# Kernel tuning notes

Hardware: AMD Instinct MI355X
Metric: run time of the kernel (lower is better)

Reference implementation:

```python
import jax, jax.numpy as jnp
import numpy as np

DT_MIN, DT_MAX = 1e-3, 0.1
DT_RANK, D_STATE = 64, 16


def setup_inputs() -> dict:
    key = jax.random.key(0)
    ks = jax.random.split(key, 8)
    B, L, D_MODEL, D_INNER = 2, 4096, 1024, 2048
    s = 0.02
    return {
        "x": jax.random.normal(ks[0], (B, L, D_MODEL), jnp.float32),
        "W_in": jax.random.normal(ks[1], (D_MODEL, 2 * D_INNER), jnp.float32) * s,
        "W_xproj": jax.random.normal(ks[2], (D_INNER, DT_RANK + 2 * D_STATE), jnp.float32) * s,
        "W_dt": jax.random.normal(ks[3], (DT_RANK, D_INNER), jnp.float32) * s,
        "b_dt": jax.random.normal(ks[4], (D_INNER,), jnp.float32) * s,
        "A_log": jnp.log(jax.random.uniform(ks[5], (D_INNER, D_STATE), jnp.float32) + 0.5),
        "D": jnp.ones((D_INNER,), jnp.float32),
        "W_out": jax.random.normal(ks[6], (D_INNER, D_MODEL), jnp.float32) * s,
    }


def _selective_scan(xp, delta, A, Bm, Cm):
    # xp, delta: [B, L, d_inner]; Bm, Cm: [B, L, d_state]; A: [d_inner, d_state]
    batch, L, d_inner = xp.shape
    d_state = A.shape[1]

    def step(h, inp):
        x_t, dt_t, B_t, C_t = inp  # [B,di], [B,di], [B,ds], [B,ds]
        A_bar = 1.0 + A[None] * dt_t[..., None]            # [B, di, ds]
        B_bar = B_t[:, None, :] * dt_t[..., None]          # [B, di, ds]
        h = A_bar * h + B_bar * x_t[..., None]             # [B, di, ds]
        y_t = jnp.sum(C_t[:, None, :] * h, axis=-1)        # [B, di]
        return h, y_t

    h0 = jnp.zeros((batch, d_inner, d_state), xp.dtype)
    xs = (
        jnp.swapaxes(xp, 0, 1),
        jnp.swapaxes(delta, 0, 1),
        jnp.swapaxes(Bm, 0, 1),
        jnp.swapaxes(Cm, 0, 1),
    )
    _, ys = jax.lax.scan(step, h0, xs)  # ys: [L, B, d_inner]
    return jnp.swapaxes(ys, 0, 1)


def reference(x, W_in, W_xproj, W_dt, b_dt, A_log, D, W_out):
    xz = x @ W_in
    xp, z = jnp.split(xz, 2, axis=-1)                      # [B,L,d_inner] each
    x_dbl = xp @ W_xproj
    dlt, Bm, Cm = jnp.split(x_dbl, [DT_RANK, DT_RANK + D_STATE], axis=-1)
    delta = jnp.clip(jax.nn.softplus(dlt @ W_dt + b_dt), DT_MIN, DT_MAX)
    A = -jnp.exp(A_log)
    y = _selective_scan(xp, delta, A, Bm, Cm)
    y = y + D[None, None, :] * xp
    y = y * jax.nn.silu(z)
    return y @ W_out
```

## Files before the change

### kernel.cpp

```cpp
#include <hip/hip_runtime.h>
#include <cstdint>
#include <cstddef>

typedef unsigned short u16;
typedef __attribute__((ext_vector_type(8))) short bf16x8;
typedef __attribute__((ext_vector_type(4))) float f32x4;

__device__ __forceinline__ float bf2f(u16 u) {
  unsigned v = ((unsigned)u) << 16;
  return __builtin_bit_cast(float, v);
}
__device__ __forceinline__ u16 f2bf(float f) {
  unsigned u = __builtin_bit_cast(unsigned, f);
  u = (u + 0x7FFFu + ((u >> 16) & 1u)) >> 16;
  return (u16)u;
}

__device__ __forceinline__ void gload16(const void* g, void* l) {
  __builtin_amdgcn_global_load_lds(
      (const __attribute__((address_space(1))) void*)g,
      (__attribute__((address_space(3))) void*)l,
      16, 0, 0);
}

__device__ __forceinline__ int swz(int lb) { return lb ^ (((lb >> 7) & 7) << 4); }

__global__ __launch_bounds__(256) void f32_to_bf16_kernel(
    const float* __restrict__ in, u16* __restrict__ out, int n) {
  int i = (blockIdx.x * 256 + threadIdx.x) * 4;
  if (i < n) {
    float4 v = *(const float4*)(in + i);
    ushort4 o;
    o.x = f2bf(v.x); o.y = f2bf(v.y); o.z = f2bf(v.z); o.w = f2bf(v.w);
    *(ushort4*)(out + i) = o;
  }
}

__global__ void transpose_f32_bf16T_kernel(
    const float* __restrict__ in, u16* __restrict__ out, int R, int C) {
  __shared__ float tile[32][33];
  const int bx = blockIdx.x * 32;
  const int by = blockIdx.y * 32;
  const int tx = threadIdx.x, ty = threadIdx.y;
#pragma unroll
  for (int i = 0; i < 32; i += 8)
    tile[ty + i][tx] = in[(size_t)(by + ty + i) * C + bx + tx];
  __syncthreads();
#pragma unroll
  for (int i = 0; i < 32; i += 8)
    out[(size_t)(bx + ty + i) * R + by + tx] = f2bf(tile[tx][ty + i]);
}

template <int BN, int EPI>
__global__ __launch_bounds__(512, 2) void gemm256(
    const u16* __restrict__ Ap, const u16* __restrict__ Btp,
    int M, int N, int K, int gx,
    void* __restrict__ o0, void* __restrict__ o1) {
  constexpr int NFR = BN / 64;
  constexpr int NFH = NFR / 2;
  constexpr int B_ISS = BN / 64;
  constexpr int WN = BN / 4;
  constexpr int AREG = 32768;
  constexpr int BUFSZ = AREG + BN * 128;
  __shared__ __align__(1024) char smem[2 * BUFSZ];

  const int tid = threadIdx.x;
  const int wid = tid >> 6, lane = tid & 63;
  const int wr = wid >> 2, wc = wid & 3;
  const int l16 = lane & 15, lk = lane >> 4;

  const int nwg = gridDim.x, bid = blockIdx.x;
  const int rb = (bid & 7) * (nwg >> 3) + (bid >> 3);
  const int bx = rb % gx, by = rb / gx;
  const int m0 = by * 256, n0 = bx * BN;

  const u16* gA[4];
  const u16* gB[B_ISS];
#pragma unroll
  for (int i = 0; i < 4; ++i) {
    int lb = swz(i * 8192 + tid * 16);
    gA[i] = Ap + (size_t)(m0 + (lb >> 7)) * K + ((lb & 127) >> 1);
  }
#pragma unroll
  for (int i = 0; i < B_ISS; ++i) {
    int lb = swz(i * 8192 + tid * 16);
    gB[i] = Btp + (size_t)(n0 + (lb >> 7)) * K + ((lb & 127) >> 1);
  }

  auto stageA = [&](int kt, int h) {
    char* dst = smem + (kt & 1) * BUFSZ + (wid << 10);
    gload16(gA[2 * h] + kt * 64, dst + (2 * h) * 8192);
    gload16(gA[2 * h + 1] + kt * 64, dst + (2 * h + 1) * 8192);
  };
  auto stageB = [&](int kt, int h) {
    char* dst = smem + (kt & 1) * BUFSZ + AREG + (wid << 10);
    if constexpr (B_ISS == 4) {
      gload16(gB[2 * h] + kt * 64, dst + (2 * h) * 8192);
      gload16(gB[2 * h + 1] + kt * 64, dst + (2 * h + 1) * 8192);
    } else {
      gload16(gB[h] + kt * 64, dst + h * 8192);
    }
  };

  auto offA = [&](int f, int kk) {
    return swz((wr * 128 + f * 16 + l16) * 128 + kk * 64 + lk * 16);
  };
  auto offB = [&](int n, int kk) {
    return swz((wc * WN + n * 16 + l16) * 128 + kk * 64 + lk * 16);
  };

  f32x4 acc[8][NFR];
#pragma unroll
  for (int f = 0; f < 8; ++f)
#pragma unroll
    for (int n = 0; n < NFR; ++n) {
      f32x4 z = {0.f, 0.f, 0.f, 0.f};
      acc[f][n] = z;
    }

  const int NT = K >> 6;
  stageA(0, 0); stageA(0, 1); stageB(0, 0); stageB(0, 1);
  stageA(1, 0);
  asm volatile("s_waitcnt vmcnt(2)" ::: "memory");
  __builtin_amdgcn_s_barrier();

  for (int kt = 0; kt < NT; ++kt) {
    const char* bufA = smem + (kt & 1) * BUFSZ;
    const char* bufB = bufA + AREG;
    bf16x8 af[4][2], bh[2][NFH][2];

#pragma unroll
    for (int j = 0; j < 4; ++j)
#pragma unroll
      for (int kk = 0; kk < 2; ++kk)
        af[j][kk] = *(const bf16x8*)(bufA + offA(j, kk));
#pragma unroll
    for (int j = 0; j < NFH; ++j)
#pragma unroll
      for (int kk = 0; kk < 2; ++kk)
        bh[0][j][kk] = *(const bf16x8*)(bufB + offB(j, kk));
    if (kt + 1 < NT) stageA(kt + 1, 1);
    __builtin_amdgcn_s_barrier();
    asm volatile("s_waitcnt lgkmcnt(0)" ::: "memory");
    __builtin_amdgcn_sched_barrier(0);
    __builtin_amdgcn_s_setprio(1);
#pragma unroll
    for (int j = 0; j < 4; ++j)
#pragma unroll
      for (int n2 = 0; n2 < NFH; ++n2)
#pragma unroll
        for (int kk = 0; kk < 2; ++kk)
          acc[j][n2] = __builtin_amdgcn_mfma_f32_16x16x32_bf16(
              af[j][kk], bh[0][n2][kk], acc[j][n2], 0, 0, 0);
    __builtin_amdgcn_s_setprio(0);
    __builtin_amdgcn_s_barrier();

#pragma unroll
    for (int j = 0; j < NFH; ++j)
#pragma unroll
      for (int kk = 0; kk < 2; ++kk)
        bh[1][j][kk] = *(const bf16x8*)(bufB + offB(NFH + j, kk));
    if (kt + 1 < NT) stageB(kt + 1, 0);
    __builtin_amdgcn_s_barrier();
    asm volatile("s_waitcnt lgkmcnt(0)" ::: "memory");
    __builtin_amdgcn_sched_barrier(0);
    __builtin_amdgcn_s_setprio(1);
#pragma unroll
    for (int j = 0; j < 4; ++j)
#pragma unroll
      for (int n2 = 0; n2 < NFH; ++n2)
#pragma unroll
        for (int kk = 0; kk < 2; ++kk)
          acc[j][NFH + n2] = __builtin_amdgcn_mfma_f32_16x16x32_bf16(
              af[j][kk], bh[1][n2][kk], acc[j][NFH + n2], 0, 0, 0);
    __builtin_amdgcn_s_setprio(0);
    __builtin_amdgcn_s_barrier();

#pragma unroll
    for (int j = 0; j < 4; ++j)
#pragma unroll
      for (int kk = 0; kk < 2; ++kk)
        af[j][kk] = *(const bf16x8*)(bufA + offA(4 + j, kk));
    if (kt + 1 < NT) stageB(kt + 1, 1);
    __builtin_amdgcn_s_barrier();
    asm volatile("s_waitcnt lgkmcnt(0)" ::: "memory");
    __builtin_amdgcn_sched_barrier(0);
    __builtin_amdgcn_s_setprio(1);
#pragma unroll
    for (int j = 0; j < 4; ++j)
#pragma unroll
      for (int n2 = 0; n2 < NFH; ++n2)
#pragma unroll
        for (int kk = 0; kk < 2; ++kk)
          acc[4 + j][NFH + n2] = __builtin_amdgcn_mfma_f32_16x16x32_bf16(
              af[j][kk], bh[1][n2][kk], acc[4 + j][NFH + n2], 0, 0, 0);
    __builtin_amdgcn_s_setprio(0);
    __builtin_amdgcn_s_barrier();

    if (kt + 2 < NT) {
      stageA(kt + 2, 0);
      asm volatile("s_waitcnt vmcnt(2)" ::: "memory");
    } else if (kt + 1 < NT) {
      asm volatile("s_waitcnt vmcnt(0)" ::: "memory");
    }
    __builtin_amdgcn_s_barrier();
    __builtin_amdgcn_s_setprio(1);
#pragma unroll
    for (int j = 0; j < 4; ++j)
#pragma unroll
      for (int n2 = 0; n2 < NFH; ++n2)
#pragma unroll
        for (int kk = 0; kk < 2; ++kk)
          acc[4 + j][n2] = __builtin_amdgcn_mfma_f32_16x16x32_bf16(
              af[j][kk], bh[0][n2][kk], acc[4 + j][n2], 0, 0, 0);
    __builtin_amdgcn_s_setprio(0);
    __builtin_amdgcn_s_barrier();
  }

#pragma unroll
  for (int f = 0; f < 8; ++f) {
#pragma unroll
    for (int n = 0; n < NFR; ++n) {
#pragma unroll
      for (int rr = 0; rr < 4; ++rr) {
        const int row = m0 + wr * 128 + f * 16 + lk * 4 + rr;
        const int col = n0 + wc * WN + n * 16 + l16;
        float v = acc[f][n][rr];
        if constexpr (EPI == 0) {
          if (col < 2048) {
            ((u16*)o0)[(size_t)row * 2048 + col] = f2bf(v);
          } else {
            float sv = v / (1.f + __expf(-v));
            ((u16*)o1)[(size_t)row * 2048 + (col - 2048)] = f2bf(sv);
          }
        } else {
          ((float*)o0)[(size_t)row * (size_t)N + col] = v;
        }
      }
    }
  }
}

template <int BN, int NR, int EPI>
__global__ __launch_bounds__(256) void gemm_bt(
    const u16* __restrict__ A, const u16* __restrict__ Bt,
    int M, int N, int K, int KS,
    void* __restrict__ o0, const float* __restrict__ bias) {
  constexpr int BM = 128, BK = 32, MR = 4;
  __shared__ __align__(16) u16 As[BM * BK];
  __shared__ __align__(16) u16 Bs[BN * BK];
  const int tid = threadIdx.x;
  const int wid = tid >> 6, lane = tid & 63;
  const int wr = wid >> 1, wc = wid & 1;
  const int m0 = blockIdx.y * BM, n0 = blockIdx.x * BN;
  const int l16 = lane & 15, lk = lane >> 4;

  f32x4 acc[MR][NR];
#pragma unroll
  for (int m = 0; m < MR; ++m)
#pragma unroll
    for (int n = 0; n < NR; ++n) {
      f32x4 z = {0.f, 0.f, 0.f, 0.f};
      acc[m][n] = z;
    }

  constexpr int CH_A = (BM * BK * 2) / 1024;
  constexpr int CH_B = (BN * BK * 2) / 1024;

  const int kbeg = blockIdx.z * KS, kend = kbeg + KS;
  for (int k0 = kbeg; k0 < kend; k0 += BK) {
    for (int c = wid; c < CH_A; c += 4) {
      int off = c * 1024 + lane * 16;
      int e = off >> 1;
      int m = e >> 5, kk = e & 31;
      gload16(A + (size_t)(m0 + m) * K + (k0 + kk), (char*)As + off);
    }
    for (int c = wid; c < CH_B; c += 4) {
      int off = c * 1024 + lane * 16;
      int e = off >> 1;
      int n = e >> 5, kk = e & 31;
      gload16(Bt + (size_t)(n0 + n) * K + (k0 + kk), (char*)Bs + off);
    }
    __syncthreads();
    bf16x8 af[MR], bfr[NR];
#pragma unroll
    for (int m = 0; m < MR; ++m)
      af[m] = *(const bf16x8*)(As + (wr * 64 + m * 16 + l16) * BK + lk * 8);
#pragma unroll
    for (int n = 0; n < NR; ++n)
      bfr[n] = *(const bf16x8*)(Bs + (wc * (NR * 16) + n * 16 + l16) * BK + lk * 8);
#pragma unroll
    for (int m = 0; m < MR; ++m)
#pragma unroll
      for (int n = 0; n < NR; ++n)
        acc[m][n] = __builtin_amdgcn_mfma_f32_16x16x32_bf16(af[m], bfr[n], acc[m][n], 0, 0, 0);
    __syncthreads();
  }

#pragma unroll
  for (int m = 0; m < MR; ++m) {
#pragma unroll
    for (int n = 0; n < NR; ++n) {
#pragma unroll
      for (int r = 0; r < 4; ++r) {
        const int row = m0 + wr * 64 + m * 16 + (lane >> 4) * 4 + r;
        const int col = n0 + wc * (NR * 16) + n * 16 + (lane & 15);
        float v = acc[m][n][r];
        if constexpr (EPI == 2) {
          v += bias[col];
          float sp = (v > 20.f) ? v : log1pf(__expf(v));
          sp = fminf(fmaxf(sp, 1e-3f), 0.1f);
          ((u16*)o0)[(size_t)row * 2048 + col] = f2bf(sp);
        } else {
          ((float*)o0)[((size_t)blockIdx.z * M + row) * 96 + col] = v;
        }
      }
    }
  }
}

__global__ __launch_bounds__(256) void reduce_xdbl(
    const float* __restrict__ part, u16* __restrict__ dlt,
    float* __restrict__ Bc, float* __restrict__ Cc) {
  int idx = blockIdx.x * 256 + threadIdx.x;
  int row = idx / 24, c4 = idx % 24;
  const float* p = part + (size_t)row * 96 + c4 * 4;
  f32x4 v = *(const f32x4*)p;
#pragma unroll
  for (int z = 1; z < 4; ++z)
    v += *(const f32x4*)(p + (size_t)z * 8192 * 96);
  int col = c4 * 4;
  if (col < 64) {
    ushort4 o;
    o.x = f2bf(v[0]); o.y = f2bf(v[1]); o.z = f2bf(v[2]); o.w = f2bf(v[3]);
    *(ushort4*)(dlt + (size_t)row * 64 + col) = o;
  } else if (col < 80) {
    *(f32x4*)(Bc + (size_t)row * 16 + (col - 64)) = v;
  } else {
    *(f32x4*)(Cc + (size_t)row * 16 + (col - 80)) = v;
  }
}

template <int TC>
__global__ __launch_bounds__(256) void scan_pass1(
    const u16* __restrict__ xp, const u16* __restrict__ dt,
    const float* __restrict__ Bc, const float* __restrict__ A_log,
    float* __restrict__ P, float* __restrict__ Q, int NC) {
  const int di = blockIdx.x * 256 + threadIdx.x;
  const int c = blockIdx.y, b = blockIdx.z;
  __shared__ __align__(16) float Bs[TC * 16];
  {
    const float* src = Bc + (size_t)(b * 4096 + c * TC) * 16;
    for (int i = threadIdx.x; i < TC * 4; i += 256)
      *(float4*)(Bs + i * 4) = *(const float4*)(src + i * 4);
  }
  float A[16], h[16], Pp[16];
#pragma unroll
  for (int s = 0; s < 16; ++s) {
    A[s] = -__expf(A_log[di * 16 + s]);
    h[s] = 0.f;
    Pp[s] = 1.f;
  }
  __syncthreads();
  size_t gidx = (size_t)(b * 4096 + c * TC) * 2048 + di;
  for (int t = 0; t < TC; ++t, gidx += 2048) {
    float xv = bf2f(xp[gidx]), dv = bf2f(dt[gidx]);
    float dvx = dv * xv;
#pragma unroll
    for (int q = 0; q < 4; ++q) {
      f32x4 bv = ((const f32x4*)(Bs + t * 16))[q];
#pragma unroll
      for (int j = 0; j < 4; ++j) {
        int s = q * 4 + j;
        float abar = fmaf(A[s], dv, 1.f);
        h[s] = fmaf(abar, h[s], bv[j] * dvx);
        Pp[s] *= abar;
      }
    }
  }
  const size_t obase = ((size_t)(b * NC + c) * 16) * 2048 + di;
#pragma unroll
  for (int s = 0; s < 16; ++s) {
    P[obase + (size_t)s * 2048] = Pp[s];
    Q[obase + (size_t)s * 2048] = h[s];
  }
}

__global__ __launch_bounds__(256) void scan_pass2(
    const float* __restrict__ P, const float* __restrict__ Q,
    float* __restrict__ Hin, int NC) {
  const int di = blockIdx.x * 256 + threadIdx.x;
  const int s = blockIdx.y, b = blockIdx.z;
  float hin = 0.f;
  const size_t idx0 = ((size_t)(b * NC) * 16 + s) * 2048 + di;
#pragma unroll 8
  for (int c = 0; c < NC; ++c) {
    size_t idx = idx0 + (size_t)c * (16 * 2048);
    Hin[idx] = hin;
    hin = fmaf(P[idx], hin, Q[idx]);
  }
}

template <int TC>
__global__ __launch_bounds__(256) void scan_pass3(
    const u16* __restrict__ xp, const u16* __restrict__ dt,
    const u16* __restrict__ zs, const float* __restrict__ Bc,
    const float* __restrict__ Cc, const float* __restrict__ A_log,
    const float* __restrict__ Dv, const float* __restrict__ Hin,
    u16* __restrict__ Y, int NC) {
  const int di = blockIdx.x * 256 + threadIdx.x;
  const int c = blockIdx.y, b = blockIdx.z;
  __shared__ __align__(16) float Bs[TC * 16], Cs[TC * 16];
  {
    const float* srcB = Bc + (size_t)(b * 4096 + c * TC) * 16;
    const float* srcC = Cc + (size_t)(b * 4096 + c * TC) * 16;
    for (int i = threadIdx.x; i < TC * 4; i += 256) {
      *(float4*)(Bs + i * 4) = *(const float4*)(srcB + i * 4);
      *(float4*)(Cs + i * 4) = *(const float4*)(srcC + i * 4);
    }
  }
  float A[16], h[16];
  const size_t hbase = ((size_t)(b * NC + c) * 16) * 2048 + di;
#pragma unroll
  for (int s = 0; s < 16; ++s) {
    A[s] = -__expf(A_log[di * 16 + s]);
    h[s] = Hin[hbase + (size_t)s * 2048];
  }
  const float Dg = Dv[di];
  __syncthreads();
  size_t gidx = (size_t)(b * 4096 + c * TC) * 2048 + di;
  for (int t = 0; t < TC; ++t, gidx += 2048) {
    float xv = bf2f(xp[gidx]), dv = bf2f(dt[gidx]), zv = bf2f(zs[gidx]);
    float dvx = dv * xv;
    float y = 0.f;
#pragma unroll
    for (int q = 0; q < 4; ++q) {
      f32x4 bv = ((const f32x4*)(Bs + t * 16))[q];
      f32x4 cv = ((const f32x4*)(Cs + t * 16))[q];
#pragma unroll
      for (int j = 0; j < 4; ++j) {
        int s = q * 4 + j;
        float abar = fmaf(A[s], dv, 1.f);
        h[s] = fmaf(abar, h[s], bv[j] * dvx);
        y = fmaf(cv[j], h[s], y);
      }
    }
    float yo = fmaf(Dg, xv, y) * zv;
    Y[gidx] = f2bf(yo);
  }
}

extern "C" void kernel_launch(void* const* d_in, const int* in_sizes, int n_in,
                              void* d_out, int out_size, void* d_ws, size_t ws_size,
                              hipStream_t stream) {
  (void)in_sizes; (void)n_in; (void)out_size; (void)ws_size;
  const float* x       = (const float*)d_in[0];
  const float* W_in    = (const float*)d_in[1];
  const float* W_xproj = (const float*)d_in[2];
  const float* W_dt    = (const float*)d_in[3];
  const float* b_dt    = (const float*)d_in[4];
  const float* A_log   = (const float*)d_in[5];
  const float* Dv      = (const float*)d_in[6];
  const float* W_out   = (const float*)d_in[7];
  float* out = (float*)d_out;

  constexpr size_t MB = 1ull << 20;
  char* ws = (char*)d_ws;
  constexpr size_t O_XP    = 0;
  constexpr size_t O_ZS    = 32 * MB;
  constexpr size_t O_DELTA = 64 * MB;
  constexpr size_t O_BC    = 96 * MB;
  constexpr size_t O_CC    = O_BC + 512 * 1024;
  constexpr size_t O_WOUTT = 97 * MB;
  constexpr size_t O_Y     = 101 * MB;
  constexpr size_t O_XB    = 133 * MB;
  constexpr size_t O_WINT  = 149 * MB;
  constexpr size_t O_WXT   = 157 * MB;
  constexpr size_t O_WDTT  = O_WXT + 393216;
  constexpr size_t O_DLT   = O_WDTT + 262144;
  constexpr size_t O_P     = 133 * MB;
  constexpr size_t O_Q     = 149 * MB;
  constexpr size_t O_HIN   = 165 * MB;
  constexpr size_t O_XDP   = O_P;

  u16* xb    = (u16*)(ws + O_XB);
  u16* WinT  = (u16*)(ws + O_WINT);
  u16* WxT   = (u16*)(ws + O_WXT);
  u16* WdtT  = (u16*)(ws + O_WDTT);
  u16* WoutT = (u16*)(ws + O_WOUTT);
  u16* xpb   = (u16*)(ws + O_XP);
  u16* zsb   = (u16*)(ws + O_ZS);
  u16* dltb  = (u16*)(ws + O_DLT);
  float* Bcf = (float*)(ws + O_BC);
  float* Ccf = (float*)(ws + O_CC);
  u16* delb  = (u16*)(ws + O_DELTA);
  u16* Yb    = (u16*)(ws + O_Y);
  float* Pf  = (float*)(ws + O_P);
  float* Qf  = (float*)(ws + O_Q);
  float* Hin = (float*)(ws + O_HIN);
  float* xdp = (float*)(ws + O_XDP);

  dim3 tb(32, 8);
  f32_to_bf16_kernel<<<8192 * 1024 / 1024, 256, 0, stream>>>(x, xb, 8192 * 1024);
  transpose_f32_bf16T_kernel<<<dim3(4096 / 32, 1024 / 32), tb, 0, stream>>>(W_in, WinT, 1024, 4096);
  transpose_f32_bf16T_kernel<<<dim3(96 / 32, 2048 / 32), tb, 0, stream>>>(W_xproj, WxT, 2048, 96);
  transpose_f32_bf16T_kernel<<<dim3(2048 / 32, 64 / 32), tb, 0, stream>>>(W_dt, WdtT, 64, 2048);
  transpose_f32_bf16T_kernel<<<dim3(1024 / 32, 2048 / 32), tb, 0, stream>>>(W_out, WoutT, 2048, 1024);

  gemm256<256, 0><<<512, 512, 0, stream>>>(
      xb, WinT, 8192, 4096, 1024, 16, xpb, zsb);
  gemm_bt<96, 3, 4><<<dim3(1, 8192 / 128, 4), 256, 0, stream>>>(
      xpb, WxT, 8192, 96, 2048, 512, xdp, nullptr);
  reduce_xdbl<<<8192 * 24 / 256, 256, 0, stream>>>(xdp, dltb, Bcf, Ccf);
  gemm_bt<128, 4, 2><<<dim3(2048 / 128, 8192 / 128, 1), 256, 0, stream>>>(
      dltb, WdtT, 8192, 2048, 64, 64, delb, b_dt);

  constexpr int NC = 64, TC = 64;
  scan_pass1<TC><<<dim3(8, NC, 2), 256, 0, stream>>>(
      xpb, delb, Bcf, A_log, Pf, Qf, NC);
  scan_pass2<<<dim3(8, 16, 2), 256, 0, stream>>>(Pf, Qf, Hin, NC);
  scan_pass3<TC><<<dim3(8, NC, 2), 256, 0, stream>>>(
      xpb, delb, zsb, Bcf, Ccf, A_log, Dv, Hin, Yb, NC);

  gemm256<128, 3><<<256, 512, 0, stream>>>(
      Yb, WoutT, 8192, 1024, 2048, 8, out, nullptr);
}
```

Baseline: 329.9 us.

## Reorganize GEMM LDS staging so tile halves load as independent groups

Remaps the A and B tile rows in shared memory so each half of the tile (A row groups, B column halves) is loaded as a separate group. The prefetch schedule changes so the next tile's first halves are issued early and second halves later, with vmcnt waits placed after the MFMA phases rather than in a separate stage. The intent is finer-grained overlap of global-to-LDS loads with compute and the removal of one barrier per iteration. The risk is that the new row interleaving and wait counts must exactly match the issue order, or the kernel will read stale data.

```diff
diff --git a/kernel.cpp b/kernel.cpp
--- a/kernel.cpp
+++ b/kernel.cpp
@@ -59,9 +59,12 @@
   constexpr int NFR = BN / 64;
   constexpr int NFH = NFR / 2;
   constexpr int B_ISS = BN / 64;
+  constexpr int BH = B_ISS / 2;
   constexpr int WN = BN / 4;
+  constexpr int HSH = (BN == 256) ? 5 : 4;
   constexpr int AREG = 32768;
-  constexpr int BUFSZ = AREG + BN * 128;
+  constexpr int BREG = BN * 128;
+  constexpr int BUFSZ = AREG + BREG;
   __shared__ __align__(1024) char smem[2 * BUFSZ];
 
   const int tid = threadIdx.x;
@@ -84,29 +87,31 @@
 #pragma unroll
   for (int i = 0; i < B_ISS; ++i) {
     int lb = swz(i * 8192 + tid * 16);
-    gB[i] = Btp + (size_t)(n0 + (lb >> 7)) * K + ((lb & 127) >> 1);
+    int rl = lb >> 7;
+    int half = (rl >= BN / 2) ? 1 : 0;
+    int r = rl & (BN / 2 - 1);
+    int n = ((r >> HSH) << (HSH + 1)) + (half << HSH) + (r & ((1 << HSH) - 1));
+    gB[i] = Btp + (size_t)(n0 + n) * K + ((lb & 127) >> 1);
   }
 
   auto stageA = [&](int kt, int h) {
     char* dst = smem + (kt & 1) * BUFSZ + (wid << 10);
-    gload16(gA[2 * h] + kt * 64, dst + (2 * h) * 8192);
-    gload16(gA[2 * h + 1] + kt * 64, dst + (2 * h + 1) * 8192);
+    gload16(gA[h] + kt * 64, dst + h * 8192);
+    gload16(gA[h + 2] + kt * 64, dst + (h + 2) * 8192);
   };
   auto stageB = [&](int kt, int h) {
     char* dst = smem + (kt & 1) * BUFSZ + AREG + (wid << 10);
-    if constexpr (B_ISS == 4) {
-      gload16(gB[2 * h] + kt * 64, dst + (2 * h) * 8192);
-      gload16(gB[2 * h + 1] + kt * 64, dst + (2 * h + 1) * 8192);
-    } else {
-      gload16(gB[h] + kt * 64, dst + h * 8192);
-    }
+#pragma unroll
+    for (int j = 0; j < BH; ++j)
+      gload16(gB[h * BH + j] + kt * 64, dst + (h * BH + j) * 8192);
   };
 
   auto offA = [&](int f, int kk) {
     return swz((wr * 128 + f * 16 + l16) * 128 + kk * 64 + lk * 16);
   };
-  auto offB = [&](int n, int kk) {
-    return swz((wc * WN + n * 16 + l16) * 128 + kk * 64 + lk * 16);
+  auto offB = [&](int nf, int kk) {
+    int rl = (nf >= NFH ? BN / 2 : 0) + wc * (WN / 2) + (nf % NFH) * 16 + l16;
+    return swz(rl * 128 + kk * 64 + lk * 16);
   };
 
   f32x4 acc[8][NFR];
@@ -119,9 +124,9 @@
     }
 
   const int NT = K >> 6;
-  stageA(0, 0); stageA(0, 1); stageB(0, 0); stageB(0, 1);
-  stageA(1, 0);
-  asm volatile("s_waitcnt vmcnt(2)" ::: "memory");
+  stageA(0, 0); stageB(0, 0); stageA(0, 1); stageB(0, 1);
+  if constexpr (BH == 2) asm volatile("s_waitcnt vmcnt(4)" ::: "memory");
+  else                   asm volatile("s_waitcnt vmcnt(3)" ::: "memory");
   __builtin_amdgcn_s_barrier();
 
   for (int kt = 0; kt < NT; ++kt) {
@@ -139,7 +144,7 @@
 #pragma unroll
       for (int kk = 0; kk < 2; ++kk)
         bh[0][j][kk] = *(const bf16x8*)(bufB + offB(j, kk));
-    if (kt + 1 < NT) stageA(kt + 1, 1);
+    if (kt + 1 < NT) stageA(kt + 1, 0);
     __builtin_amdgcn_s_barrier();
     asm volatile("s_waitcnt lgkmcnt(0)" ::: "memory");
     __builtin_amdgcn_sched_barrier(0);
@@ -153,6 +158,8 @@
           acc[j][n2] = __builtin_amdgcn_mfma_f32_16x16x32_bf16(
               af[j][kk], bh[0][n2][kk], acc[j][n2], 0, 0, 0);
     __builtin_amdgcn_s_setprio(0);
+    if (kt + 1 < NT) asm volatile("s_waitcnt vmcnt(2)" ::: "memory");
+    else             asm volatile("s_waitcnt vmcnt(0)" ::: "memory");
     __builtin_amdgcn_s_barrier();
 
 #pragma unroll
@@ -181,7 +188,7 @@
 #pragma unroll
       for (int kk = 0; kk < 2; ++kk)
         af[j][kk] = *(const bf16x8*)(bufA + offA(4 + j, kk));
-    if (kt + 1 < NT) stageB(kt + 1, 1);
+    if (kt + 1 < NT) { stageA(kt + 1, 1); stageB(kt + 1, 1); }
     __builtin_amdgcn_s_barrier();
     asm volatile("s_waitcnt lgkmcnt(0)" ::: "memory");
     __builtin_amdgcn_sched_barrier(0);
@@ -197,13 +204,6 @@
     __builtin_amdgcn_s_setprio(0);
     __builtin_amdgcn_s_barrier();
 
-    if (kt + 2 < NT) {
-      stageA(kt + 2, 0);
-      asm volatile("s_waitcnt vmcnt(2)" ::: "memory");
-    } else if (kt + 1 < NT) {
-      asm volatile("s_waitcnt vmcnt(0)" ::: "memory");
-    }
-    __builtin_amdgcn_s_barrier();
     __builtin_amdgcn_s_setprio(1);
 #pragma unroll
     for (int j = 0; j < 4; ++j)
@@ -214,6 +214,10 @@
           acc[4 + j][n2] = __builtin_amdgcn_mfma_f32_16x16x32_bf16(
               af[j][kk], bh[0][n2][kk], acc[4 + j][n2], 0, 0, 0);
     __builtin_amdgcn_s_setprio(0);
+    if (kt + 1 < NT) {
+      if constexpr (BH == 2) asm volatile("s_waitcnt vmcnt(4)" ::: "memory");
+      else                   asm volatile("s_waitcnt vmcnt(3)" ::: "memory");
+    }
     __builtin_amdgcn_s_barrier();
   }
 
```

New measurement: 328.0 us. No clear change (-0.6%).

## Load GEMM B operand directly to registers and single-buffer A in LDS

Applied to the files above, without the earlier changes.

The gemm256 kernel stops staging the B (weight) tile through LDS. Each wave now loads its B fragments straight from global memory into registers, ping-ponged across two register sets by unrolling the k loop by two. A is single-buffered in a 32KB LDS region with split staging and new vmcnt waits, and block rasterization changes to column-major over M tiles (gy). This cuts LDS footprint and LDS traffic, but adds register pressure and uncoalesced-ish global loads for B, and it assumes NT is even.

```diff
diff --git a/kernel.cpp b/kernel.cpp
--- a/kernel.cpp
+++ b/kernel.cpp
@@ -54,15 +54,13 @@
 template <int BN, int EPI>
 __global__ __launch_bounds__(512, 2) void gemm256(
     const u16* __restrict__ Ap, const u16* __restrict__ Btp,
-    int M, int N, int K, int gx,
+    int M, int N, int K, int gy,
     void* __restrict__ o0, void* __restrict__ o1) {
   constexpr int NFR = BN / 64;
   constexpr int NFH = NFR / 2;
-  constexpr int B_ISS = BN / 64;
+  constexpr int BL = 2 * NFH;
   constexpr int WN = BN / 4;
-  constexpr int AREG = 32768;
-  constexpr int BUFSZ = AREG + BN * 128;
-  __shared__ __align__(1024) char smem[2 * BUFSZ];
+  __shared__ __align__(1024) char smem[32768];
 
   const int tid = threadIdx.x;
   const int wid = tid >> 6, lane = tid & 63;
@@ -71,43 +69,31 @@
 
   const int nwg = gridDim.x, bid = blockIdx.x;
   const int rb = (bid & 7) * (nwg >> 3) + (bid >> 3);
-  const int bx = rb % gx, by = rb / gx;
+  const int by = rb % gy, bx = rb / gy;
   const int m0 = by * 256, n0 = bx * BN;
 
-  const u16* gA[4];
-  const u16* gB[B_ISS];
+  unsigned aoff[4];
 #pragma unroll
   for (int i = 0; i < 4; ++i) {
     int lb = swz(i * 8192 + tid * 16);
-    gA[i] = Ap + (size_t)(m0 + (lb >> 7)) * K + ((lb & 127) >> 1);
-  }
-#pragma unroll
-  for (int i = 0; i < B_ISS; ++i) {
-    int lb = swz(i * 8192 + tid * 16);
-    gB[i] = Btp + (size_t)(n0 + (lb >> 7)) * K + ((lb & 127) >> 1);
-  }
-
+    aoff[i] = (unsigned)(m0 + (lb >> 7)) * K + ((lb & 127) >> 1);
+  }
   auto stageA = [&](int kt, int h) {
-    char* dst = smem + (kt & 1) * BUFSZ + (wid << 10);
-    gload16(gA[2 * h] + kt * 64, dst + (2 * h) * 8192);
-    gload16(gA[2 * h + 1] + kt * 64, dst + (2 * h + 1) * 8192);
+    char* dst = smem + (wid << 10);
+    gload16(Ap + aoff[h] + kt * 64, dst + h * 8192);
+    gload16(Ap + aoff[h + 2] + kt * 64, dst + (h + 2) * 8192);
   };
-  auto stageB = [&](int kt, int h) {
-    char* dst = smem + (kt & 1) * BUFSZ + AREG + (wid << 10);
-    if constexpr (B_ISS == 4) {
-      gload16(gB[2 * h] + kt * 64, dst + (2 * h) * 8192);
-      gload16(gB[2 * h + 1] + kt * 64, dst + (2 * h + 1) * 8192);
-    } else {
-      gload16(gB[h] + kt * 64, dst + h * 8192);
-    }
-  };
-
   auto offA = [&](int f, int kk) {
     return swz((wr * 128 + f * 16 + l16) * 128 + kk * 64 + lk * 16);
   };
-  auto offB = [&](int n, int kk) {
-    return swz((wc * WN + n * 16 + l16) * 128 + kk * 64 + lk * 16);
-  };
+
+  unsigned boff[2][NFH];
+#pragma unroll
+  for (int h = 0; h < 2; ++h)
+#pragma unroll
+    for (int nf = 0; nf < NFH; ++nf)
+      boff[h][nf] =
+          (unsigned)(n0 + wc * WN + (h * NFH + nf) * 16 + l16) * K + lk * 8;
 
   f32x4 acc[8][NFR];
 #pragma unroll
@@ -118,28 +104,31 @@
       acc[f][n] = z;
     }
 
+  bf16x8 bhX[2][NFH][2], bhY[2][NFH][2];
+  auto loadB = [&](bf16x8 (&dst)[2][NFH][2], int h, int kt) {
+#pragma unroll
+    for (int nf = 0; nf < NFH; ++nf)
+#pragma unroll
+      for (int kk = 0; kk < 2; ++kk)
+        dst[h][nf][kk] =
+            *(const bf16x8*)(Btp + boff[h][nf] + kt * 64 + kk * 32);
+  };
+
   const int NT = K >> 6;
-  stageA(0, 0); stageA(0, 1); stageB(0, 0); stageB(0, 1);
-  stageA(1, 0);
-  asm volatile("s_waitcnt vmcnt(2)" ::: "memory");
+
+  stageA(0, 0); stageA(0, 1);
+  loadB(bhX, 0, 0); loadB(bhX, 1, 0);
+  asm volatile("s_waitcnt vmcnt(0)" ::: "memory");
   __builtin_amdgcn_s_barrier();
 
-  for (int kt = 0; kt < NT; ++kt) {
-    const char* bufA = smem + (kt & 1) * BUFSZ;
-    const char* bufB = bufA + AREG;
-    bf16x8 af[4][2], bh[2][NFH][2];
-
+  auto body = [&](int kt, bf16x8 (&cur)[2][NFH][2],
+                  bf16x8 (&nxt)[2][NFH][2], bool hasnext) {
+    bf16x8 af[4][2];
 #pragma unroll
     for (int j = 0; j < 4; ++j)
 #pragma unroll
       for (int kk = 0; kk < 2; ++kk)
-        af[j][kk] = *(const bf16x8*)(bufA + offA(j, kk));
-#pragma unroll
-    for (int j = 0; j < NFH; ++j)
-#pragma unroll
-      for (int kk = 0; kk < 2; ++kk)
-        bh[0][j][kk] = *(const bf16x8*)(bufB + offB(j, kk));
-    if (kt + 1 < NT) stageA(kt + 1, 1);
+        af[j][kk] = *(const bf16x8*)(smem + offA(j, kk));
     __builtin_amdgcn_s_barrier();
     asm volatile("s_waitcnt lgkmcnt(0)" ::: "memory");
     __builtin_amdgcn_sched_barrier(0);
@@ -151,16 +140,35 @@
 #pragma unroll
         for (int kk = 0; kk < 2; ++kk)
           acc[j][n2] = __builtin_amdgcn_mfma_f32_16x16x32_bf16(
-              af[j][kk], bh[0][n2][kk], acc[j][n2], 0, 0, 0);
+              af[j][kk], cur[0][n2][kk], acc[j][n2], 0, 0, 0);
     __builtin_amdgcn_s_setprio(0);
     __builtin_amdgcn_s_barrier();
 
-#pragma unroll
-    for (int j = 0; j < NFH; ++j)
+    if (hasnext) stageA(kt + 1, 0);
+    __builtin_amdgcn_s_setprio(1);
+#pragma unroll
+    for (int j = 0; j < 4; ++j)
+#pragma unroll
+      for (int n2 = 0; n2 < NFH; ++n2)
+#pragma unroll
+        for (int kk = 0; kk < 2; ++kk)
+          acc[j][NFH + n2] = __builtin_amdgcn_mfma_f32_16x16x32_bf16(
+              af[j][kk], cur[1][n2][kk], acc[j][NFH + n2], 0, 0, 0);
+    __builtin_amdgcn_s_setprio(0);
+    if (hasnext) {
+      if constexpr (BL == 4) asm volatile("s_waitcnt vmcnt(6)" ::: "memory");
+      else                   asm volatile("s_waitcnt vmcnt(4)" ::: "memory");
+    } else {
+      asm volatile("s_waitcnt vmcnt(0)" ::: "memory");
+    }
+    __builtin_amdgcn_s_barrier();
+
+#pragma unroll
+    for (int j = 0; j < 4; ++j)
 #pragma unroll
       for (int kk = 0; kk < 2; ++kk)
-        bh[1][j][kk] = *(const bf16x8*)(bufB + offB(NFH + j, kk));
-    if (kt + 1 < NT) stageB(kt + 1, 0);
+        af[j][kk] = *(const bf16x8*)(smem + offA(4 + j, kk));
+    if (hasnext) loadB(nxt, 0, kt + 1);
     __builtin_amdgcn_s_barrier();
     asm volatile("s_waitcnt lgkmcnt(0)" ::: "memory");
     __builtin_amdgcn_sched_barrier(0);
@@ -171,39 +179,12 @@
       for (int n2 = 0; n2 < NFH; ++n2)
 #pragma unroll
         for (int kk = 0; kk < 2; ++kk)
-          acc[j][NFH + n2] = __builtin_amdgcn_mfma_f32_16x16x32_bf16(
-              af[j][kk], bh[1][n2][kk], acc[j][NFH + n2], 0, 0, 0);
+          acc[4 + j][NFH + n2] = __builtin_amdgcn_mfma_f32_16x16x32_bf16(
+              af[j][kk], cur[1][n2][kk], acc[4 + j][NFH + n2], 0, 0, 0);
     __builtin_amdgcn_s_setprio(0);
     __builtin_amdgcn_s_barrier();
 
-#pragma unroll
-    for (int j = 0; j < 4; ++j)
-#pragma unroll
-      for (int kk = 0; kk < 2; ++kk)
-        af[j][kk] = *(const bf16x8*)(bufA + offA(4 + j, kk));
-    if (kt + 1 < NT) stageB(kt + 1, 1);
-    __builtin_amdgcn_s_barrier();
-    asm volatile("s_waitcnt lgkmcnt(0)" ::: "memory");
-    __builtin_amdgcn_sched_barrier(0);
-    __builtin_amdgcn_s_setprio(1);
-#pragma unroll
-    for (int j = 0; j < 4; ++j)
-#pragma unroll
-      for (int n2 = 0; n2 < NFH; ++n2)
-#pragma unroll
-        for (int kk = 0; kk < 2; ++kk)
-          acc[4 + j][NFH + n2] = __builtin_amdgcn_mfma_f32_16x16x32_bf16(
-              af[j][kk], bh[1][n2][kk], acc[4 + j][NFH + n2], 0, 0, 0);
-    __builtin_amdgcn_s_setprio(0);
-    __builtin_amdgcn_s_barrier();
-
-    if (kt + 2 < NT) {
-      stageA(kt + 2, 0);
-      asm volatile("s_waitcnt vmcnt(2)" ::: "memory");
-    } else if (kt + 1 < NT) {
-      asm volatile("s_waitcnt vmcnt(0)" ::: "memory");
-    }
-    __builtin_amdgcn_s_barrier();
+    if (hasnext) { stageA(kt + 1, 1); loadB(nxt, 1, kt + 1); }
     __builtin_amdgcn_s_setprio(1);
 #pragma unroll
     for (int j = 0; j < 4; ++j)
@@ -212,9 +193,18 @@
 #pragma unroll
         for (int kk = 0; kk < 2; ++kk)
           acc[4 + j][n2] = __builtin_amdgcn_mfma_f32_16x16x32_bf16(
-              af[j][kk], bh[0][n2][kk], acc[4 + j][n2], 0, 0, 0);
+              af[j][kk], cur[0][n2][kk], acc[4 + j][n2], 0, 0, 0);
     __builtin_amdgcn_s_setprio(0);
+    if (hasnext) {
+      if constexpr (BL == 4) asm volatile("s_waitcnt vmcnt(10)" ::: "memory");
+      else                   asm volatile("s_waitcnt vmcnt(6)" ::: "memory");
+    }
     __builtin_amdgcn_s_barrier();
+  };
+
+  for (int kt = 0; kt < NT; kt += 2) {
+    body(kt, bhX, bhY, true);
+    body(kt + 1, bhY, bhX, kt + 2 < NT);
   }
 
 #pragma unroll
@@ -508,7 +498,7 @@
   transpose_f32_bf16T_kernel<<<dim3(1024 / 32, 2048 / 32), tb, 0, stream>>>(W_out, WoutT, 2048, 1024);
 
   gemm256<256, 0><<<512, 512, 0, stream>>>(
-      xb, WinT, 8192, 4096, 1024, 16, xpb, zsb);
+      xb, WinT, 8192, 4096, 1024, 32, xpb, zsb);
   gemm_bt<96, 3, 4><<<dim3(1, 8192 / 128, 4), 256, 0, stream>>>(
       xpb, WxT, 8192, 96, 2048, 512, xdp, nullptr);
   reduce_xdbl<<<8192 * 24 / 256, 256, 0, stream>>>(xdp, dltb, Bcf, Ccf);
@@ -523,5 +513,5 @@
       xpb, delb, zsb, Bcf, Ccf, A_log, Dv, Hin, Yb, NC);
 
   gemm256<128, 3><<<256, 512, 0, stream>>>(
-      Yb, WoutT, 8192, 1024, 2048, 8, out, nullptr);
-}
+      Yb, WoutT, 8192, 1024, 2048, 32, out, nullptr);
+}
```

New measurement: 442.6 us. 1.34x slower.
